# Kernel tuning notes

Hardware: AMD Instinct MI355X
Metric: run time of the kernel (lower is better)

The kernel has to match this reference:

```python
import jax, jax.numpy as jnp
import numpy as np

EXP_EMBD = 1024
EXP_Q_H = 8
EXP_HEAD_DIM = 256
EXP_KV_H = 1
EXP_KV_DIM = EXP_KV_H * EXP_HEAD_DIM  # 256
EXP_FFN = 4096
B, L, LC = 8, 512, 2048


def setup_inputs() -> dict:
    key = jax.random.key(0)
    ks = jax.random.split(key, 12)
    def w(k, shape):
        fan_in = shape[-1]
        return jax.random.normal(k, shape, jnp.float32) * (fan_in ** -0.5)
    return {
        "x": jax.random.normal(ks[0], (B, L, EXP_EMBD), jnp.float32),
        "text_k": jax.random.normal(ks[1], (B, LC, EXP_KV_DIM), jnp.float32),
        "text_v": jax.random.normal(ks[2], (B, LC, EXP_KV_DIM), jnp.float32),
        "ln1_w": jnp.ones((EXP_EMBD,), jnp.float32),
        "ln2_w": jnp.ones((EXP_EMBD,), jnp.float32),
        "Wq": w(ks[3], (EXP_Q_H * EXP_HEAD_DIM, EXP_EMBD)),
        "Wk": w(ks[4], (EXP_KV_DIM, EXP_KV_DIM)),
        "Wv": w(ks[5], (EXP_KV_DIM, EXP_KV_DIM)),
        "Wo": w(ks[6], (EXP_EMBD, EXP_Q_H * EXP_HEAD_DIM)),
        "Wg": w(ks[7], (EXP_FFN, EXP_EMBD)),
        "Wu": w(ks[8], (EXP_FFN, EXP_EMBD)),
        "Wd": w(ks[9], (EXP_EMBD, EXP_FFN)),
    }


def _rmsnorm(x, w):
    # torch.nn.RMSNorm with eps=None -> eps = finfo(dtype).eps
    eps = jnp.asarray(jnp.finfo(jnp.float32).eps, x.dtype)
    return x * jax.lax.rsqrt(jnp.mean(x * x, axis=-1, keepdims=True) + eps) * w


def _rope(x):
    # x: [B, L, H, D]
    b, l, h, d = x.shape
    d2 = d // 2
    ts = 10000.0 ** (2.0 / d * jnp.arange(d2, dtype=jnp.float32))  # [d2]
    rad = jnp.arange(l, dtype=jnp.float32)[:, None] / ts[None, :]  # [L, d2]
    s = jnp.sin(rad)[None, :, None, :]
    c = jnp.cos(rad)[None, :, None, :]
    x1, x2 = x[..., :d2], x[..., d2:]
    return jnp.concatenate([x1 * c - x2 * s, x2 * c + x1 * s], axis=-1)


def reference(x, text_k, text_v, ln1_w, ln2_w, Wq, Wk, Wv, Wo, Wg, Wu, Wd):
    b, l, _ = x.shape
    lc = text_k.shape[1]
    residual = x
    h = _rmsnorm(x, ln1_w)
    q = _rope((h @ Wq.T).reshape(b, l, EXP_Q_H, EXP_HEAD_DIM))          # [B,L,QH,D]
    k = (text_k @ Wk.T).reshape(b, lc, EXP_KV_H, EXP_HEAD_DIM)          # [B,Lc,KVH,D]
    v = (text_v @ Wv.T).reshape(b, lc, EXP_KV_H, EXP_HEAD_DIM)
    kv_map = (jnp.arange(EXP_Q_H) * EXP_KV_H) // EXP_Q_H                # GQA head map
    kh = jnp.take(k, kv_map, axis=2)                                    # [B,Lc,QH,D]
    vh = jnp.take(v, kv_map, axis=2)
    scale = 1.0 / np.sqrt(EXP_HEAD_DIM).astype(np.float32)
    scores = jnp.einsum('blhd,bchd->bhlc', q, kh) * scale               # [B,QH,L,Lc]
    attn = jax.nn.softmax(scores, axis=-1)
    ctx = jnp.einsum('bhlc,bchd->blhd', attn, vh).reshape(b, l, -1)
    x = ctx @ Wo.T + residual
    residual = x
    h = _rmsnorm(x, ln2_w)
    return (jax.nn.silu(h @ Wg.T) * (h @ Wu.T)) @ Wd.T + residual
```

## Files before the change

### kernel.cpp

```cpp
#include <hip/hip_runtime.h>

typedef __attribute__((ext_vector_type(4))) float f32x4;
typedef __attribute__((ext_vector_type(8))) short s16x8;
typedef __attribute__((ext_vector_type(4))) unsigned short u16x4;

#define B_    8
#define L_    512
#define LC_   2048
#define EMBD  1024

__device__ __forceinline__ float b2f(unsigned short u) {
  unsigned int i = ((unsigned int)u) << 16;
  float f; __builtin_memcpy(&f, &i, 4); return f;
}
__device__ __forceinline__ unsigned short f2b(float f) {
  unsigned int i; __builtin_memcpy(&i, &f, 4);
  unsigned int r = i + 0x7FFFu + ((i >> 16) & 1u);
  return (unsigned short)(r >> 16);
}

#define GLL16(g, l)                                                         \
  __builtin_amdgcn_global_load_lds(                                         \
      (__attribute__((address_space(1))) void*)(g),                         \
      (__attribute__((address_space(3))) void*)(l), 16, 0, 0)

#define VMCNT6() asm volatile("s_waitcnt vmcnt(6)" ::: "memory")
#define VMCNT0() asm volatile("s_waitcnt vmcnt(0)" ::: "memory")
#define LGKM0()  asm volatile("s_waitcnt lgkmcnt(0)" ::: "memory")

__global__ __launch_bounds__(256) void convert_f32_bf16(
    const float* __restrict__ in, unsigned short* __restrict__ out, int n4) {
  int i = blockIdx.x * 256 + threadIdx.x;
  if (i >= n4) return;
  float4 v = ((const float4*)in)[i];
  u16x4 o = { f2b(v.x), f2b(v.y), f2b(v.z), f2b(v.w) };
  ((u16x4*)out)[i] = o;
}

__global__ __launch_bounds__(256) void rmsnorm_kernel(
    const float* __restrict__ x, const float* __restrict__ w,
    unsigned short* __restrict__ out) {
  int row = blockIdx.x;
  int tid = threadIdx.x;
  float4 v = ((const float4*)(x + (size_t)row * EMBD))[tid];
  float ss = v.x*v.x + v.y*v.y + v.z*v.z + v.w*v.w;
#pragma unroll
  for (int o = 1; o < 64; o <<= 1) ss += __shfl_xor(ss, o);
  __shared__ float red[4];
  if ((tid & 63) == 0) red[tid >> 6] = ss;
  __syncthreads();
  float tot = red[0] + red[1] + red[2] + red[3];
  float rs = rsqrtf(tot * (1.0f / EMBD) + 1.1920928955078125e-07f);
  float4 wv = ((const float4*)w)[tid];
  u16x4 o = { f2b(v.x*rs*wv.x), f2b(v.y*rs*wv.y), f2b(v.z*rs*wv.z), f2b(v.w*rs*wv.w) };
  ((u16x4*)(out + (size_t)row * EMBD))[tid] = o;
}

__global__ __launch_bounds__(256) void rope_kernel(unsigned short* __restrict__ q) {
  int idx = blockIdx.x * 256 + threadIdx.x;
  int i   = idx & 127;
  int h   = (idx >> 7) & 7;
  int row = idx >> 10;
  int l   = row & (L_ - 1);
  size_t base = (size_t)row * 2048 + h * 256 + i;
  float x1 = b2f(q[base]);
  float x2 = b2f(q[base + 128]);
  float ts  = powf(10000.0f, (float)i * (2.0f / 256.0f));
  float rad = (float)l / ts;
  float s, c;
  sincosf(rad, &s, &c);
  q[base]       = f2b(x1 * c - x2 * s);
  q[base + 128] = f2b(x2 * c + x1 * s);
}

__global__ __launch_bounds__(256) void act_kernel(
    const unsigned short* __restrict__ g, const unsigned short* __restrict__ u,
    unsigned short* __restrict__ out, int n8) {
  int i = blockIdx.x * 256 + threadIdx.x;
  if (i >= n8) return;
  s16x8 gv = ((const s16x8*)g)[i];
  s16x8 uv = ((const s16x8*)u)[i];
  s16x8 ov;
#pragma unroll
  for (int j = 0; j < 8; ++j) {
    float gf = b2f((unsigned short)gv[j]);
    float uf = b2f((unsigned short)uv[j]);
    float s  = gf / (1.0f + __expf(-gf));
    ov[j] = (short)f2b(s * uf);
  }
  ((s16x8*)out)[i] = ov;
}

template <int ADD_RES, int OUT_BF16>
__global__ __launch_bounds__(256, 2) void gemm_nt(
    const unsigned short* __restrict__ A, const unsigned short* __restrict__ Bw,
    const float* __restrict__ Res, void* __restrict__ C, int M, int N, int K) {
  __shared__ unsigned short As[128 * 64];
  __shared__ unsigned short Bs[128 * 64];
  const int tid = threadIdx.x;
  const int lane = tid & 63, wid = tid >> 6;
  const int l15 = lane & 15, l4 = lane >> 4;
  const int wr = wid >> 1, wc = wid & 1;
  const int m0 = blockIdx.y * 128, n0 = blockIdx.x * 128;

  const f32x4 fz = {0.f, 0.f, 0.f, 0.f};
  f32x4 acc[4][4];
#pragma unroll
  for (int i = 0; i < 4; ++i)
#pragma unroll
    for (int j = 0; j < 4; ++j) acc[i][j] = fz;

  for (int k0 = 0; k0 < K; k0 += 64) {
    __syncthreads();
#pragma unroll
    for (int i = 0; i < 4; ++i) {
      int Li = i * 4096 + tid * 16;
      int row = Li >> 7;
      int kb = (Li & 127) ^ ((row & 7) << 4);
      GLL16((const char*)(A + (size_t)(m0 + row) * K + k0) + kb, (char*)As + Li);
      GLL16((const char*)(Bw + (size_t)(n0 + row) * K + k0) + kb, (char*)Bs + Li);
    }
    __syncthreads();
#pragma unroll
    for (int kk = 0; kk < 2; ++kk) {
      s16x8 af[4], bfr[4];
#pragma unroll
      for (int mi = 0; mi < 4; ++mi) {
        int row = wr * 64 + mi * 16 + l15;
        int kb = (kk * 64 + l4 * 16) ^ ((row & 7) << 4);
        af[mi] = *(const s16x8*)((const char*)As + row * 128 + kb);
      }
#pragma unroll
      for (int ni = 0; ni < 4; ++ni) {
        int row = wc * 64 + ni * 16 + l15;
        int kb = (kk * 64 + l4 * 16) ^ ((row & 7) << 4);
        bfr[ni] = *(const s16x8*)((const char*)Bs + row * 128 + kb);
      }
#pragma unroll
      for (int mi = 0; mi < 4; ++mi)
#pragma unroll
        for (int ni = 0; ni < 4; ++ni)
          acc[mi][ni] = __builtin_amdgcn_mfma_f32_16x16x32_bf16(
              af[mi], bfr[ni], acc[mi][ni], 0, 0, 0);
    }
  }
#pragma unroll
  for (int mi = 0; mi < 4; ++mi) {
#pragma unroll
    for (int r = 0; r < 4; ++r) {
      int grow = m0 + wr * 64 + mi * 16 + l4 * 4 + r;
      size_t base = (size_t)grow * N + n0 + wc * 64 + l15;
#pragma unroll
      for (int ni = 0; ni < 4; ++ni) {
        float v = acc[mi][ni][r];
        size_t idx = base + ni * 16;
        if (ADD_RES) v += Res[idx];
        if (OUT_BF16) ((unsigned short*)C)[idx] = f2b(v);
        else          ((float*)C)[idx] = v;
      }
    }
  }
}

__global__ __launch_bounds__(512, 2) void gemm256(
    const unsigned short* __restrict__ A, const unsigned short* __restrict__ Bw,
    unsigned short* __restrict__ C, int M, int N, int K) {
  extern __shared__ char smem[];
  const int tid = threadIdx.x;
  const int lane = tid & 63;
  const int wid = tid >> 6;
  const int wr = wid >> 2, wc = wid & 3;
  const int l15 = lane & 15, g = lane >> 4;
  int flat = blockIdx.y * 16 + blockIdx.x;
  flat = (flat & 7) * 32 + (flat >> 3);
  const int m0 = (flat >> 4) * 256, n0 = (flat & 15) * 256;
  const int T = K >> 6;
  const int swz = (l15 & 7) << 4;

  auto stage = [&](int t, int mat, int half) {
    char* dst = smem + mat * 65536 + (t & 1) * 32768 + half * 16384;
    const unsigned short* src = (mat ? Bw + (size_t)(n0 + half * 128) * K
                                     : A + (size_t)(m0 + half * 128) * K) + t * 64;
#pragma unroll
    for (int i = 0; i < 2; ++i) {
      int Li = i * 8192 + tid * 16;
      int row = Li >> 7;
      int kb = (Li & 127) ^ ((row & 7) << 4);
      GLL16((const char*)(src + (size_t)row * K) + kb, dst + Li);
    }
  };

  const f32x4 fz = {0.f, 0.f, 0.f, 0.f};
  f32x4 acc[2][2][4][2];
#pragma unroll
  for (int ms = 0; ms < 2; ++ms)
#pragma unroll
    for (int ns = 0; ns < 2; ++ns)
#pragma unroll
      for (int mi = 0; mi < 4; ++mi)
#pragma unroll
        for (int ni = 0; ni < 2; ++ni) acc[ms][ns][mi][ni] = fz;

  stage(0, 1, 0); stage(0, 1, 1); stage(0, 0, 0); stage(0, 0, 1);
  stage(1, 1, 0); stage(1, 1, 1); stage(1, 0, 0);
  VMCNT6();
  __builtin_amdgcn_s_barrier();

  for (int t = 0; t < T; ++t) {
    char* Ab = smem + (t & 1) * 32768 + wr * 16384;
    char* Bb = smem + 65536 + (t & 1) * 32768 + (wc >> 1) * 16384;
    const int bn = (wc & 1) * 64;
    s16x8 a[4][2], b0[2][2], b1[2][2];

#pragma unroll
    for (int mi = 0; mi < 4; ++mi) {
      int row = mi * 16 + l15;
#pragma unroll
      for (int kk = 0; kk < 2; ++kk)
        a[mi][kk] = *(const s16x8*)(Ab + row * 128 + ((kk * 64 + g * 16) ^ swz));
    }
#pragma unroll
    for (int ni = 0; ni < 2; ++ni) {
      int r0 = (bn + ni * 16 + l15) * 128;
      int r1 = (bn + 32 + ni * 16 + l15) * 128;
#pragma unroll
      for (int kk = 0; kk < 2; ++kk) {
        int ko = (kk * 64 + g * 16) ^ swz;
        b0[ni][kk] = *(const s16x8*)(Bb + r0 + ko);
        b1[ni][kk] = *(const s16x8*)(Bb + r1 + ko);
      }
    }
    if (t + 1 < T) stage(t + 1, 0, 1);
    __builtin_amdgcn_s_barrier();
    LGKM0();
    __builtin_amdgcn_sched_barrier(0);
    __builtin_amdgcn_s_setprio(1);
#pragma unroll
    for (int mi = 0; mi < 4; ++mi)
#pragma unroll
      for (int ni = 0; ni < 2; ++ni)
#pragma unroll
        for (int kk = 0; kk < 2; ++kk)
          acc[0][0][mi][ni] = __builtin_amdgcn_mfma_f32_16x16x32_bf16(
              a[mi][kk], b0[ni][kk], acc[0][0][mi][ni], 0, 0, 0);
    __builtin_amdgcn_s_setprio(0);
    __builtin_amdgcn_s_barrier();

    if (t + 2 < T) stage(t + 2, 1, 0);
    __builtin_amdgcn_s_barrier();
    __builtin_amdgcn_s_setprio(1);
#pragma unroll
    for (int mi = 0; mi < 4; ++mi)
#pragma unroll
      for (int ni = 0; ni < 2; ++ni)
#pragma unroll
        for (int kk = 0; kk < 2; ++kk)
          acc[0][1][mi][ni] = __builtin_amdgcn_mfma_f32_16x16x32_bf16(
              a[mi][kk], b1[ni][kk], acc[0][1][mi][ni], 0, 0, 0);
    __builtin_amdgcn_s_setprio(0);
    __builtin_amdgcn_s_barrier();

#pragma unroll
    for (int mi = 0; mi < 4; ++mi) {
      int row = 64 + mi * 16 + l15;
#pragma unroll
      for (int kk = 0; kk < 2; ++kk)
        a[mi][kk] = *(const s16x8*)(Ab + row * 128 + ((kk * 64 + g * 16) ^ swz));
    }
    if (t + 2 < T) stage(t + 2, 1, 1);
    __builtin_amdgcn_s_barrier();
    LGKM0();
    __builtin_amdgcn_sched_barrier(0);
    __builtin_amdgcn_s_setprio(1);
#pragma unroll
    for (int mi = 0; mi < 4; ++mi)
#pragma unroll
      for (int ni = 0; ni < 2; ++ni)
#pragma unroll
        for (int kk = 0; kk < 2; ++kk)
          acc[1][0][mi][ni] = __builtin_amdgcn_mfma_f32_16x16x32_bf16(
              a[mi][kk], b0[ni][kk], acc[1][0][mi][ni], 0, 0, 0);
    __builtin_amdgcn_s_setprio(0);
    __builtin_amdgcn_s_barrier();

    if (t + 2 < T) { stage(t + 2, 0, 0); VMCNT6(); }
    else           { VMCNT0(); }
    __builtin_amdgcn_s_barrier();
    __builtin_amdgcn_s_setprio(1);
#pragma unroll
    for (int mi = 0; mi < 4; ++mi)
#pragma unroll
      for (int ni = 0; ni < 2; ++ni)
#pragma unroll
        for (int kk = 0; kk < 2; ++kk)
          acc[1][1][mi][ni] = __builtin_amdgcn_mfma_f32_16x16x32_bf16(
              a[mi][kk], b1[ni][kk], acc[1][1][mi][ni], 0, 0, 0);
    __builtin_amdgcn_s_setprio(0);
    __builtin_amdgcn_s_barrier();
  }

#pragma unroll
  for (int ms = 0; ms < 2; ++ms)
#pragma unroll
    for (int mi = 0; mi < 4; ++mi)
#pragma unroll
      for (int r = 0; r < 4; ++r) {
        int grow = m0 + wr * 128 + ms * 64 + mi * 16 + g * 4 + r;
        size_t base = (size_t)grow * N + n0 + wc * 64;
#pragma unroll
        for (int ns = 0; ns < 2; ++ns)
#pragma unroll
          for (int ni = 0; ni < 2; ++ni)
            C[base + ns * 32 + ni * 16 + l15] = f2b(acc[ms][ns][mi][ni][r]);
      }
}

#define SWZV(d) (((((d) & 7) ^ (((d) >> 3) & 7))) << 4)

__global__ __launch_bounds__(512, 2) void attn_kernel(
    const unsigned short* __restrict__ Q,
    const unsigned short* __restrict__ Kc,
    const unsigned short* __restrict__ Vc,
    unsigned short* __restrict__ Ctx) {
  __shared__ unsigned short Ks[64 * 256];
  __shared__ unsigned short Vt[256 * 64];
  const int tid = threadIdx.x;
  const int lane = tid & 63, wid = tid >> 6;
  const int l15 = lane & 15, g = lane >> 4;
  const int qt = blockIdx.x, h = blockIdx.y, b = blockIdx.z;

  const size_t qrow = (size_t)(b * L_ + qt * 128 + wid * 16 + l15);
  const unsigned short* qp = Q + qrow * 2048 + h * 256;
  s16x8 qf[8];
#pragma unroll
  for (int kc = 0; kc < 8; ++kc) qf[kc] = *(const s16x8*)(qp + kc * 32 + g * 8);

  const f32x4 fz = {0.f, 0.f, 0.f, 0.f};
  f32x4 oacc[16];
#pragma unroll
  for (int i = 0; i < 16; ++i) oacc[i] = fz;
  float m_run = -__builtin_inff(), l_run = 0.f;

  const unsigned short* Kb = Kc + (size_t)b * LC_ * 256;
  const unsigned short* Vb = Vc + (size_t)b * LC_ * 256;

  for (int kt = 0; kt < LC_ / 64; ++kt) {
    __syncthreads();
#pragma unroll
    for (int i = 0; i < 4; ++i) {
      int Li = i * 8192 + tid * 16;
      int row = Li >> 9;
      int kb = (Li & 511) ^ ((row & 7) << 4);
      GLL16((const char*)(Kb + (size_t)(kt * 64 + row) * 256) + kb, (char*)Ks + Li);
    }
#pragma unroll
    for (int p = 0; p < 2; ++p) {
      int id = p * 512 + tid;
      int dgrp = id & 31;
      int kvp = id >> 5;
      int d0 = dgrp * 8, kv0 = kvp * 2;
      const unsigned short* v0p = Vb + (size_t)(kt * 64 + kv0) * 256 + d0;
      s16x8 r0 = *(const s16x8*)v0p;
      s16x8 r1 = *(const s16x8*)(v0p + 256);
#pragma unroll
      for (int j = 0; j < 8; ++j) {
        int d = d0 + j;
        unsigned int val = (unsigned int)(unsigned short)r0[j] |
                           ((unsigned int)(unsigned short)r1[j] << 16);
        *(unsigned int*)((char*)Vt + d * 128 + ((kv0 * 2) ^ SWZV(d))) = val;
      }
    }
    __syncthreads();

    f32x4 sacc[4];
#pragma unroll
    for (int mi = 0; mi < 4; ++mi) sacc[mi] = fz;
#pragma unroll
    for (int mi = 0; mi < 4; ++mi) {
      int row = mi * 16 + l15;
      int swz = (row & 7) << 4;
#pragma unroll
      for (int kc = 0; kc < 8; ++kc) {
        s16x8 kf = *(const s16x8*)((const char*)Ks + row * 512 + ((kc * 64 + g * 16) ^ swz));
        sacc[mi] = __builtin_amdgcn_mfma_f32_16x16x32_bf16(kf, qf[kc], sacc[mi], 0, 0, 0);
      }
    }
    float sv[4][4];
    float mt = -__builtin_inff();
#pragma unroll
    for (int mi = 0; mi < 4; ++mi)
#pragma unroll
      for (int r = 0; r < 4; ++r) {
        float t = sacc[mi][r] * 0.0625f;
        sv[mi][r] = t;
        mt = fmaxf(mt, t);
      }
    mt = fmaxf(mt, __shfl_xor(mt, 16));
    mt = fmaxf(mt, __shfl_xor(mt, 32));
    float mnew = fmaxf(m_run, mt);
    float alpha = __expf(m_run - mnew);
    float rs = 0.f;
#pragma unroll
    for (int mi = 0; mi < 4; ++mi)
#pragma unroll
      for (int r = 0; r < 4; ++r) {
        float p = __expf(sv[mi][r] - mnew);
        sv[mi][r] = p;
        rs += p;
      }
    rs += __shfl_xor(rs, 16);
    rs += __shfl_xor(rs, 32);
    l_run = l_run * alpha + rs;
    m_run = mnew;
    float af4[4];
#pragma unroll
    for (int r = 0; r < 4; ++r) af4[r] = __shfl(alpha, g * 4 + r);
#pragma unroll
    for (int nd = 0; nd < 16; ++nd)
#pragma unroll
      for (int r = 0; r < 4; ++r) oacc[nd][r] *= af4[r];
    unsigned int pk[4][2];
#pragma unroll
    for (int ni = 0; ni < 4; ++ni) {
      pk[ni][0] = (unsigned int)f2b(sv[ni][0]) | ((unsigned int)f2b(sv[ni][1]) << 16);
      pk[ni][1] = (unsigned int)f2b(sv[ni][2]) | ((unsigned int)f2b(sv[ni][3]) << 16);
    }
    int cbase = (g & 1) << 3;
#pragma unroll
    for (int t = 0; t < 2; ++t) {
      unsigned int w[4];
#pragma unroll
      for (int jj = 0; jj < 4; ++jj) {
        int c = cbase + (jj << 1);
        int src = ((c >> 2) << 4) + l15;
        unsigned int ra = __shfl(pk[2 * t][jj & 1], src);
        unsigned int rb = __shfl(pk[2 * t + 1][jj & 1], src);
        w[jj] = (g < 2) ? ra : rb;
      }
      union { unsigned int u[4]; s16x8 v; } cvt;
      cvt.u[0] = w[0]; cvt.u[1] = w[1]; cvt.u[2] = w[2]; cvt.u[3] = w[3];
      s16x8 ap = cvt.v;
#pragma unroll
      for (int nd = 0; nd < 16; ++nd) {
        int d = nd * 16 + l15;
        s16x8 vf = *(const s16x8*)((const char*)Vt + d * 128 + ((t * 64 + g * 16) ^ SWZV(d)));
        oacc[nd] = __builtin_amdgcn_mfma_f32_16x16x32_bf16(ap, vf, oacc[nd], 0, 0, 0);
      }
    }
  }
  float lf[4];
#pragma unroll
  for (int r = 0; r < 4; ++r) lf[r] = 1.0f / __shfl(l_run, g * 4 + r);
  const size_t orow0 = (size_t)(b * L_ + qt * 128 + wid * 16);
#pragma unroll
  for (int r = 0; r < 4; ++r) {
    size_t base = (orow0 + g * 4 + r) * 2048 + h * 256 + l15;
#pragma unroll
    for (int nd = 0; nd < 16; ++nd)
      Ctx[base + nd * 16] = f2b(oacc[nd][r] * lf[r]);
  }
}

extern "C" void kernel_launch(void* const* d_in, const int* in_sizes, int n_in,
                              void* d_out, int out_size, void* d_ws, size_t ws_size,
                              hipStream_t stream) {
  const float* x   = (const float*)d_in[0];
  const float* tk  = (const float*)d_in[1];
  const float* tv  = (const float*)d_in[2];
  const float* ln1 = (const float*)d_in[3];
  const float* ln2 = (const float*)d_in[4];
  const float* Wq  = (const float*)d_in[5];
  const float* Wk  = (const float*)d_in[6];
  const float* Wv  = (const float*)d_in[7];
  const float* Wo  = (const float*)d_in[8];
  const float* Wg  = (const float*)d_in[9];
  const float* Wu  = (const float*)d_in[10];
  const float* Wd  = (const float*)d_in[11];
  float* out = (float*)d_out;
  char* ws = (char*)d_ws;

  (void)hipFuncSetAttribute((const void*)gemm256,
                            hipFuncAttributeMaxDynamicSharedMemorySize, 131072);

  unsigned short* tk_bf  = (unsigned short*)(ws + 0);
  unsigned short* tv_bf  = (unsigned short*)(ws + 8388608);
  unsigned short* k_bf   = (unsigned short*)(ws + 16777216);
  unsigned short* v_bf   = (unsigned short*)(ws + 25165824);
  unsigned short* g_bf   = (unsigned short*)(ws + 0);
  unsigned short* q_bf   = (unsigned short*)(ws + 33554432);
  unsigned short* ctx_bf = (unsigned short*)(ws + 50331648);
  unsigned short* u_bf   = (unsigned short*)(ws + 33554432);
  unsigned short* wq_bf  = (unsigned short*)(ws + 67108864);
  unsigned short* wk_bf  = (unsigned short*)(ws + 71303168);
  unsigned short* wv_bf  = (unsigned short*)(ws + 71434240);
  unsigned short* wo_bf  = (unsigned short*)(ws + 71565312);
  unsigned short* wg_bf  = (unsigned short*)(ws + 75759616);
  unsigned short* wu_bf  = (unsigned short*)(ws + 84148224);
  unsigned short* wd_bf  = (unsigned short*)(ws + 92536832);
  unsigned short* h_bf   = (unsigned short*)(ws + 100925440);
  float*          x2     = (float*)(ws + 109314048);

  dim3 blk(256);
  auto cvt = [&](const float* src, unsigned short* dst, int n) {
    convert_f32_bf16<<<dim3(n / 1024), blk, 0, stream>>>(src, dst, n / 4);
  };
  cvt(Wq, wq_bf, 2097152);
  cvt(Wk, wk_bf, 65536);
  cvt(Wv, wv_bf, 65536);
  cvt(Wo, wo_bf, 2097152);
  cvt(Wg, wg_bf, 4194304);
  cvt(Wu, wu_bf, 4194304);
  cvt(Wd, wd_bf, 4194304);
  cvt(tk, tk_bf, 4194304);
  cvt(tv, tv_bf, 4194304);

  rmsnorm_kernel<<<dim3(4096), blk, 0, stream>>>(x, ln1, h_bf);
  gemm_nt<0, 1><<<dim3(16, 32), blk, 0, stream>>>(h_bf, wq_bf, nullptr, q_bf, 4096, 2048, 1024);
  rope_kernel<<<dim3(16384), blk, 0, stream>>>(q_bf);
  gemm_nt<0, 1><<<dim3(2, 128), blk, 0, stream>>>(tk_bf, wk_bf, nullptr, k_bf, 16384, 256, 256);
  gemm_nt<0, 1><<<dim3(2, 128), blk, 0, stream>>>(tv_bf, wv_bf, nullptr, v_bf, 16384, 256, 256);
  attn_kernel<<<dim3(4, 8, 8), dim3(512), 0, stream>>>(q_bf, k_bf, v_bf, ctx_bf);
  gemm_nt<1, 0><<<dim3(8, 32), blk, 0, stream>>>(ctx_bf, wo_bf, x, x2, 4096, 1024, 2048);
  rmsnorm_kernel<<<dim3(4096), blk, 0, stream>>>(x2, ln2, h_bf);
  gemm256<<<dim3(16, 16), dim3(512), 131072, stream>>>(h_bf, wg_bf, g_bf, 4096, 4096, 1024);
  gemm256<<<dim3(16, 16), dim3(512), 131072, stream>>>(h_bf, wu_bf, u_bf, 4096, 4096, 1024);
  act_kernel<<<dim3(8192), blk, 0, stream>>>(g_bf, u_bf, g_bf, 2097152);
  gemm_nt<1, 0><<<dim3(8, 32), blk, 0, stream>>>(g_bf, wd_bf, x2, out, 4096, 1024, 4096);
}
```

Baseline: 435.2 us.

## Split attention KV range, add lazy rescale, smaller GEMM tiles, fuse conversions

Merges the nine f32->bf16 conversion launches into one kernel. Splits attention over two halves of the key sequence, doubling the grid, and adds a merge kernel that combines the partial outputs with their (max, sum) statistics. The online softmax now rescales only when the running max grows by more than a threshold. The out-projection, down-projection and K/V projections use a new 64x128-tile GEMM so more blocks fill the device. The changes add extra workspace traffic for the partial outputs and a merge launch, and they also rely on workspace buffers aliasing correctly.

```diff
diff --git a/kernel.cpp b/kernel.cpp
--- a/kernel.cpp
+++ b/kernel.cpp
@@ -28,13 +28,28 @@
 #define VMCNT0() asm volatile("s_waitcnt vmcnt(0)" ::: "memory")
 #define LGKM0()  asm volatile("s_waitcnt lgkmcnt(0)" ::: "memory")
 
-__global__ __launch_bounds__(256) void convert_f32_bf16(
-    const float* __restrict__ in, unsigned short* __restrict__ out, int n4) {
-  int i = blockIdx.x * 256 + threadIdx.x;
-  if (i >= n4) return;
-  float4 v = ((const float4*)in)[i];
+__global__ __launch_bounds__(256) void convert9(
+    const float* s0, const float* s1, const float* s2, const float* s3,
+    const float* s4, const float* s5, const float* s6, const float* s7,
+    const float* s8,
+    unsigned short* d0, unsigned short* d1, unsigned short* d2,
+    unsigned short* d3, unsigned short* d4, unsigned short* d5,
+    unsigned short* d6, unsigned short* d7, unsigned short* d8) {
+  int bk = blockIdx.x;
+  const float* s; unsigned short* d; int base;
+  if      (bk <  2048) { s = s0; d = d0; base = 0; }
+  else if (bk <  2112) { s = s1; d = d1; base = 2048; }
+  else if (bk <  2176) { s = s2; d = d2; base = 2112; }
+  else if (bk <  4224) { s = s3; d = d3; base = 2176; }
+  else if (bk <  8320) { s = s4; d = d4; base = 4224; }
+  else if (bk < 12416) { s = s5; d = d5; base = 8320; }
+  else if (bk < 16512) { s = s6; d = d6; base = 12416; }
+  else if (bk < 20608) { s = s7; d = d7; base = 16512; }
+  else                 { s = s8; d = d8; base = 20608; }
+  int i = (bk - base) * 256 + threadIdx.x;
+  float4 v = ((const float4*)s)[i];
   u16x4 o = { f2b(v.x), f2b(v.y), f2b(v.z), f2b(v.w) };
-  ((u16x4*)out)[i] = o;
+  ((u16x4*)d)[i] = o;
 }
 
 __global__ __launch_bounds__(256) void rmsnorm_kernel(
@@ -162,6 +177,83 @@
   }
 }
 
+template <int ADD_RES, int OUT_BF16>
+__global__ __launch_bounds__(256, 2) void gemm_nt64(
+    const unsigned short* __restrict__ A, const unsigned short* __restrict__ Bw,
+    const float* __restrict__ Res, void* __restrict__ C, int M, int N, int K) {
+  __shared__ unsigned short As[64 * 64];
+  __shared__ unsigned short Bs[128 * 64];
+  const int tid = threadIdx.x;
+  const int lane = tid & 63, wid = tid >> 6;
+  const int l15 = lane & 15, l4 = lane >> 4;
+  const int wr = wid >> 1, wc = wid & 1;
+  const int m0 = blockIdx.y * 64, n0 = blockIdx.x * 128;
+
+  const f32x4 fz = {0.f, 0.f, 0.f, 0.f};
+  f32x4 acc[2][4];
+#pragma unroll
+  for (int i = 0; i < 2; ++i)
+#pragma unroll
+    for (int j = 0; j < 4; ++j) acc[i][j] = fz;
+
+  for (int k0 = 0; k0 < K; k0 += 64) {
+    __syncthreads();
+#pragma unroll
+    for (int i = 0; i < 2; ++i) {
+      int Li = i * 4096 + tid * 16;
+      int row = Li >> 7;
+      int kb = (Li & 127) ^ ((row & 7) << 4);
+      GLL16((const char*)(A + (size_t)(m0 + row) * K + k0) + kb, (char*)As + Li);
+    }
+#pragma unroll
+    for (int i = 0; i < 4; ++i) {
+      int Li = i * 4096 + tid * 16;
+      int row = Li >> 7;
+      int kb = (Li & 127) ^ ((row & 7) << 4);
+      GLL16((const char*)(Bw + (size_t)(n0 + row) * K + k0) + kb, (char*)Bs + Li);
+    }
+    __syncthreads();
+#pragma unroll
+    for (int kk = 0; kk < 2; ++kk) {
+      s16x8 af[2], bfr[4];
+#pragma unroll
+      for (int mi = 0; mi < 2; ++mi) {
+        int row = wr * 32 + mi * 16 + l15;
+        int kb = (kk * 64 + l4 * 16) ^ ((row & 7) << 4);
+        af[mi] = *(const s16x8*)((const char*)As + row * 128 + kb);
+      }
+#pragma unroll
+      for (int ni = 0; ni < 4; ++ni) {
+        int row = wc * 64 + ni * 16 + l15;
+        int kb = (kk * 64 + l4 * 16) ^ ((row & 7) << 4);
+        bfr[ni] = *(const s16x8*)((const char*)Bs + row * 128 + kb);
+      }
+#pragma unroll
+      for (int mi = 0; mi < 2; ++mi)
+#pragma unroll
+        for (int ni = 0; ni < 4; ++ni)
+          acc[mi][ni] = __builtin_amdgcn_mfma_f32_16x16x32_bf16(
+              af[mi], bfr[ni], acc[mi][ni], 0, 0, 0);
+    }
+  }
+#pragma unroll
+  for (int mi = 0; mi < 2; ++mi) {
+#pragma unroll
+    for (int r = 0; r < 4; ++r) {
+      int grow = m0 + wr * 32 + mi * 16 + l4 * 4 + r;
+      size_t base = (size_t)grow * N + n0 + wc * 64 + l15;
+#pragma unroll
+      for (int ni = 0; ni < 4; ++ni) {
+        float v = acc[mi][ni][r];
+        size_t idx = base + ni * 16;
+        if (ADD_RES) v += Res[idx];
+        if (OUT_BF16) ((unsigned short*)C)[idx] = f2b(v);
+        else          ((float*)C)[idx] = v;
+      }
+    }
+  }
+}
+
 __global__ __launch_bounds__(512, 2) void gemm256(
     const unsigned short* __restrict__ A, const unsigned short* __restrict__ Bw,
     unsigned short* __restrict__ C, int M, int N, int K) {
@@ -321,13 +413,15 @@
     const unsigned short* __restrict__ Q,
     const unsigned short* __restrict__ Kc,
     const unsigned short* __restrict__ Vc,
-    unsigned short* __restrict__ Ctx) {
+    unsigned short* __restrict__ Op0, unsigned short* __restrict__ Op1,
+    float2* __restrict__ Ml0, float2* __restrict__ Ml1) {
   __shared__ unsigned short Ks[64 * 256];
   __shared__ unsigned short Vt[256 * 64];
   const int tid = threadIdx.x;
   const int lane = tid & 63, wid = tid >> 6;
   const int l15 = lane & 15, g = lane >> 4;
-  const int qt = blockIdx.x, h = blockIdx.y, b = blockIdx.z;
+  const int qt = blockIdx.x, h = blockIdx.y;
+  const int b = blockIdx.z >> 1, half = blockIdx.z & 1;
 
   const size_t qrow = (size_t)(b * L_ + qt * 128 + wid * 16 + l15);
   const unsigned short* qp = Q + qrow * 2048 + h * 256;
@@ -344,7 +438,8 @@
   const unsigned short* Kb = Kc + (size_t)b * LC_ * 256;
   const unsigned short* Vb = Vc + (size_t)b * LC_ * 256;
 
-  for (int kt = 0; kt < LC_ / 64; ++kt) {
+  const int kt0 = half * 16;
+  for (int kt = kt0; kt < kt0 + 16; ++kt) {
     __syncthreads();
 #pragma unroll
     for (int i = 0; i < 4; ++i) {
@@ -397,28 +492,31 @@
       }
     mt = fmaxf(mt, __shfl_xor(mt, 16));
     mt = fmaxf(mt, __shfl_xor(mt, 32));
-    float mnew = fmaxf(m_run, mt);
-    float alpha = __expf(m_run - mnew);
+    if (!__all(mt <= m_run + 8.0f)) {
+      float mnew = fmaxf(m_run, mt);
+      float alpha = __expf(m_run - mnew);
+      float af4[4];
+#pragma unroll
+      for (int r = 0; r < 4; ++r) af4[r] = __shfl(alpha, g * 4 + r);
+#pragma unroll
+      for (int nd = 0; nd < 16; ++nd)
+#pragma unroll
+        for (int r = 0; r < 4; ++r) oacc[nd][r] *= af4[r];
+      l_run *= alpha;
+      m_run = mnew;
+    }
     float rs = 0.f;
 #pragma unroll
     for (int mi = 0; mi < 4; ++mi)
 #pragma unroll
       for (int r = 0; r < 4; ++r) {
-        float p = __expf(sv[mi][r] - mnew);
+        float p = __expf(sv[mi][r] - m_run);
         sv[mi][r] = p;
         rs += p;
       }
     rs += __shfl_xor(rs, 16);
     rs += __shfl_xor(rs, 32);
-    l_run = l_run * alpha + rs;
-    m_run = mnew;
-    float af4[4];
-#pragma unroll
-    for (int r = 0; r < 4; ++r) af4[r] = __shfl(alpha, g * 4 + r);
-#pragma unroll
-    for (int nd = 0; nd < 16; ++nd)
-#pragma unroll
-      for (int r = 0; r < 4; ++r) oacc[nd][r] *= af4[r];
+    l_run += rs;
     unsigned int pk[4][2];
 #pragma unroll
     for (int ni = 0; ni < 4; ++ni) {
@@ -427,14 +525,14 @@
     }
     int cbase = (g & 1) << 3;
 #pragma unroll
-    for (int t = 0; t < 2; ++t) {
+    for (int tt = 0; tt < 2; ++tt) {
       unsigned int w[4];
 #pragma unroll
       for (int jj = 0; jj < 4; ++jj) {
         int c = cbase + (jj << 1);
         int src = ((c >> 2) << 4) + l15;
-        unsigned int ra = __shfl(pk[2 * t][jj & 1], src);
-        unsigned int rb = __shfl(pk[2 * t + 1][jj & 1], src);
+        unsigned int ra = __shfl(pk[2 * tt][jj & 1], src);
+        unsigned int rb = __shfl(pk[2 * tt + 1][jj & 1], src);
         w[jj] = (g < 2) ? ra : rb;
       }
       union { unsigned int u[4]; s16x8 v; } cvt;
@@ -443,11 +541,13 @@
 #pragma unroll
       for (int nd = 0; nd < 16; ++nd) {
         int d = nd * 16 + l15;
-        s16x8 vf = *(const s16x8*)((const char*)Vt + d * 128 + ((t * 64 + g * 16) ^ SWZV(d)));
+        s16x8 vf = *(const s16x8*)((const char*)Vt + d * 128 + ((tt * 64 + g * 16) ^ SWZV(d)));
         oacc[nd] = __builtin_amdgcn_mfma_f32_16x16x32_bf16(ap, vf, oacc[nd], 0, 0, 0);
       }
     }
   }
+  unsigned short* Op = half ? Op1 : Op0;
+  float2* Ml = half ? Ml1 : Ml0;
   float lf[4];
 #pragma unroll
   for (int r = 0; r < 4; ++r) lf[r] = 1.0f / __shfl(l_run, g * 4 + r);
@@ -457,8 +557,32 @@
     size_t base = (orow0 + g * 4 + r) * 2048 + h * 256 + l15;
 #pragma unroll
     for (int nd = 0; nd < 16; ++nd)
-      Ctx[base + nd * 16] = f2b(oacc[nd][r] * lf[r]);
-  }
+      Op[base + nd * 16] = f2b(oacc[nd][r] * lf[r]);
+  }
+  if (g == 0) Ml[(orow0 + l15) * 8 + h] = make_float2(m_run, l_run);
+}
+
+__global__ __launch_bounds__(256) void attn_merge(
+    const unsigned short* __restrict__ p0, const unsigned short* __restrict__ p1,
+    const float2* __restrict__ ml0, const float2* __restrict__ ml1,
+    unsigned short* __restrict__ ctx) {
+  int i = blockIdx.x * 256 + threadIdx.x;
+  int rowh = i >> 5;
+  int dch = i & 31;
+  float2 a = ml0[rowh], c = ml1[rowh];
+  float M = fmaxf(a.x, c.x);
+  float w0 = a.y * __expf(a.x - M), w1 = c.y * __expf(c.x - M);
+  float inv = 1.0f / (w0 + w1);
+  w0 *= inv; w1 *= inv;
+  int row = rowh >> 3, h = rowh & 7;
+  size_t off = (size_t)row * 2048 + h * 256 + dch * 8;
+  s16x8 v0 = *(const s16x8*)(p0 + off);
+  s16x8 v1 = *(const s16x8*)(p1 + off);
+  s16x8 o;
+#pragma unroll
+  for (int j = 0; j < 8; ++j)
+    o[j] = (short)f2b(w0 * b2f((unsigned short)v0[j]) + w1 * b2f((unsigned short)v1[j]));
+  *(s16x8*)(ctx + off) = o;
 }
 
 extern "C" void kernel_launch(void* const* d_in, const int* in_sizes, int n_in,
@@ -487,6 +611,7 @@
   unsigned short* k_bf   = (unsigned short*)(ws + 16777216);
   unsigned short* v_bf   = (unsigned short*)(ws + 25165824);
   unsigned short* g_bf   = (unsigned short*)(ws + 0);
+  unsigned short* op0    = (unsigned short*)(ws + 0);
   unsigned short* q_bf   = (unsigned short*)(ws + 33554432);
   unsigned short* ctx_bf = (unsigned short*)(ws + 50331648);
   unsigned short* u_bf   = (unsigned short*)(ws + 33554432);
@@ -498,32 +623,27 @@
   unsigned short* wu_bf  = (unsigned short*)(ws + 84148224);
   unsigned short* wd_bf  = (unsigned short*)(ws + 92536832);
   unsigned short* h_bf   = (unsigned short*)(ws + 100925440);
+  float2*         ml0    = (float2*)(ws + 100925440);
+  float2*         ml1    = (float2*)(ws + 100925440 + 262144);
   float*          x2     = (float*)(ws + 109314048);
+  unsigned short* op1    = (unsigned short*)(ws + 109314048);
 
   dim3 blk(256);
-  auto cvt = [&](const float* src, unsigned short* dst, int n) {
-    convert_f32_bf16<<<dim3(n / 1024), blk, 0, stream>>>(src, dst, n / 4);
-  };
-  cvt(Wq, wq_bf, 2097152);
-  cvt(Wk, wk_bf, 65536);
-  cvt(Wv, wv_bf, 65536);
-  cvt(Wo, wo_bf, 2097152);
-  cvt(Wg, wg_bf, 4194304);
-  cvt(Wu, wu_bf, 4194304);
-  cvt(Wd, wd_bf, 4194304);
-  cvt(tk, tk_bf, 4194304);
-  cvt(tv, tv_bf, 4194304);
+  convert9<<<dim3(24704), blk, 0, stream>>>(
+      Wq, Wk, Wv, Wo, Wg, Wu, Wd, tk, tv,
+      wq_bf, wk_bf, wv_bf, wo_bf, wg_bf, wu_bf, wd_bf, tk_bf, tv_bf);
 
   rmsnorm_kernel<<<dim3(4096), blk, 0, stream>>>(x, ln1, h_bf);
   gemm_nt<0, 1><<<dim3(16, 32), blk, 0, stream>>>(h_bf, wq_bf, nullptr, q_bf, 4096, 2048, 1024);
   rope_kernel<<<dim3(16384), blk, 0, stream>>>(q_bf);
-  gemm_nt<0, 1><<<dim3(2, 128), blk, 0, stream>>>(tk_bf, wk_bf, nullptr, k_bf, 16384, 256, 256);
-  gemm_nt<0, 1><<<dim3(2, 128), blk, 0, stream>>>(tv_bf, wv_bf, nullptr, v_bf, 16384, 256, 256);
-  attn_kernel<<<dim3(4, 8, 8), dim3(512), 0, stream>>>(q_bf, k_bf, v_bf, ctx_bf);
-  gemm_nt<1, 0><<<dim3(8, 32), blk, 0, stream>>>(ctx_bf, wo_bf, x, x2, 4096, 1024, 2048);
+  gemm_nt64<0, 1><<<dim3(2, 256), blk, 0, stream>>>(tk_bf, wk_bf, nullptr, k_bf, 16384, 256, 256);
+  gemm_nt64<0, 1><<<dim3(2, 256), blk, 0, stream>>>(tv_bf, wv_bf, nullptr, v_bf, 16384, 256, 256);
+  attn_kernel<<<dim3(4, 8, 16), dim3(512), 0, stream>>>(q_bf, k_bf, v_bf, op0, op1, ml0, ml1);
+  attn_merge<<<dim3(4096), blk, 0, stream>>>(op0, op1, ml0, ml1, ctx_bf);
+  gemm_nt64<1, 0><<<dim3(8, 64), blk, 0, stream>>>(ctx_bf, wo_bf, x, x2, 4096, 1024, 2048);
   rmsnorm_kernel<<<dim3(4096), blk, 0, stream>>>(x2, ln2, h_bf);
   gemm256<<<dim3(16, 16), dim3(512), 131072, stream>>>(h_bf, wg_bf, g_bf, 4096, 4096, 1024);
   gemm256<<<dim3(16, 16), dim3(512), 131072, stream>>>(h_bf, wu_bf, u_bf, 4096, 4096, 1024);
   act_kernel<<<dim3(8192), blk, 0, stream>>>(g_bf, u_bf, g_bf, 2097152);
-  gemm_nt<1, 0><<<dim3(8, 32), blk, 0, stream>>>(g_bf, wd_bf, x2, out, 4096, 1024, 4096);
-}
+  gemm_nt64<1, 0><<<dim3(8, 64), blk, 0, stream>>>(g_bf, wd_bf, x2, out, 4096, 1024, 4096);
+}
```

New measurement: 411.6 us. 1.06x faster.
